# Kernel optimization log

Hardware: AMD Instinct MI355X
Metric: run time of the kernel (lower is better)

## Reference

```python
import jax, jax.numpy as jnp
import numpy as np

GROUPS = 32
NUM_HEADS = 8
EPS = 1e-5


def setup_inputs() -> dict:
    key = jax.random.key(0)
    ks = jax.random.split(key, 8)
    b, c, h, w = 2, 256, 64, 64
    x = jax.random.normal(ks[0], (b, c, h, w), dtype=jnp.float32)
    gn_w = jnp.ones((c,), dtype=jnp.float32)
    gn_b = jnp.zeros((c,), dtype=jnp.float32)
    qkv_w = jax.random.normal(ks[1], (3 * c, c), dtype=jnp.float32) * 0.02  # 1x1 conv
    qkv_b = jnp.zeros((3 * c,), dtype=jnp.float32)
    proj_w = jax.random.normal(ks[2], (c, c), dtype=jnp.float32) * 0.02  # 1x1 conv
    proj_b = jnp.zeros((c,), dtype=jnp.float32)
    return {"x": x, "gn_w": gn_w, "gn_b": gn_b, "qkv_w": qkv_w,
            "qkv_b": qkv_b, "proj_w": proj_w, "proj_b": proj_b}


def _group_norm(x, w, b):
    bsz, c, h, wd = x.shape
    xg = x.reshape(bsz, GROUPS, c // GROUPS, h * wd)
    mean = jnp.mean(xg, axis=(2, 3), keepdims=True)
    var = jnp.mean(jnp.square(xg - mean), axis=(2, 3), keepdims=True)
    xn = ((xg - mean) * jax.lax.rsqrt(var + EPS)).reshape(bsz, c, h, wd)
    return xn * w[None, :, None, None] + b[None, :, None, None]


def reference(x, gn_w, gn_b, qkv_w, qkv_b, proj_w, proj_b):
    b, c, h, w = x.shape
    hd = c // NUM_HEADS
    s = h * w
    xn = _group_norm(x, gn_w, gn_b)
    # 1x1 conv == channel matmul
    qkv = jnp.einsum('oc,bcs->bos', qkv_w, xn.reshape(b, c, s)) + qkv_b[None, :, None]
    qkv = qkv.reshape(b, 3, NUM_HEADS, hd, s)
    q, k, v = qkv[:, 0], qkv[:, 1], qkv[:, 2]  # (b, nh, hd, s)
    scale = 1.0 / jnp.sqrt(jnp.asarray(hd, dtype=x.dtype))
    scores = jnp.einsum('bhds,bhdt->bhst', q, k) * scale  # (b, nh, s, s)
    attn = jax.nn.softmax(scores, axis=-1)
    out = jnp.einsum('bhst,bhdt->bhds', attn, v)  # (b, nh, hd, s)
    out = out.reshape(b, c, h, w)
    out = jnp.einsum('oc,bcs->bos', proj_w, out.reshape(b, c, s)).reshape(b, c, h, w)
    out = out + proj_b[None, :, None, None]
    return out + x
```

## Files before the change

### kernel.cpp

```cpp
#include <hip/hip_runtime.h>
#include <hip/hip_bf16.h>

#define B_ 2
#define C_ 256
#define S_ 4096
#define NH 8
#define HD 32
#define EPSV 1e-5f
#define QSC2 0.25503487942324256f

typedef __bf16 bf16_t;
typedef bf16_t bf16x8 __attribute__((ext_vector_type(8)));
typedef float f32x4 __attribute__((ext_vector_type(4)));
typedef float f32x16 __attribute__((ext_vector_type(16)));
typedef int i32x2 __attribute__((ext_vector_type(2)));
typedef __hip_bfloat16 hbf;

__device__ inline unsigned cvtpk_bf16(float a, float b) {
  unsigned r;
  asm("v_cvt_pk_bf16_f32 %0, %1, %2" : "=v"(r) : "v"(a), "v"(b));
  return r;
}

#if __has_builtin(__builtin_amdgcn_exp2f)
#define EXP2R(x) __builtin_amdgcn_exp2f(x)
#else
#define EXP2R(x) exp2f(x)
#endif

__global__ __launch_bounds__(256) void f2bf_kernel(const float* __restrict__ src, hbf* __restrict__ dst, int n) {
  int i = blockIdx.x * 256 + threadIdx.x;
  if (i < n) dst[i] = __float2bfloat16(src[i]);
}

__global__ __launch_bounds__(1024) void gn_kernel(const float* __restrict__ x, const float* __restrict__ gw,
                                                  const float* __restrict__ gb, hbf* __restrict__ xn_t) {
  int b = blockIdx.x >> 5, g = blockIdx.x & 31;
  const float* xp = x + ((size_t)b * C_ + g * 8) * S_;
  float sum = 0.f, sumsq = 0.f;
  const float4* xp4 = (const float4*)xp;
  for (int i = threadIdx.x; i < 8 * S_ / 4; i += 1024) {
    float4 v = xp4[i];
    sum += v.x + v.y + v.z + v.w;
    sumsq += v.x * v.x + v.y * v.y + v.z * v.z + v.w * v.w;
  }
#pragma unroll
  for (int off = 32; off > 0; off >>= 1) {
    sum += __shfl_down(sum, off);
    sumsq += __shfl_down(sumsq, off);
  }
  __shared__ float red[2][16];
  int wid = threadIdx.x >> 6;
  if ((threadIdx.x & 63) == 0) { red[0][wid] = sum; red[1][wid] = sumsq; }
  __syncthreads();
  sum = 0.f; sumsq = 0.f;
#pragma unroll
  for (int k = 0; k < 16; k++) { sum += red[0][k]; sumsq += red[1][k]; }
  const float inv_n = 1.f / (8 * S_);
  float mean = sum * inv_n;
  float rstd = rsqrtf(fmaxf(sumsq * inv_n - mean * mean, 0.f) + EPSV);
  float scv[8], shv[8];
#pragma unroll
  for (int c = 0; c < 8; c++) {
    scv[c] = gw[g * 8 + c] * rstd;
    shv[c] = gb[g * 8 + c] - mean * scv[c];
  }
  hbf* outp = xn_t + (size_t)b * S_ * C_ + g * 8;
  for (int s = threadIdx.x; s < S_; s += 1024) {
    alignas(16) hbf tmp[8];
#pragma unroll
    for (int c = 0; c < 8; c++)
      tmp[c] = __float2bfloat16(xp[(size_t)c * S_ + s] * scv[c] + shv[c]);
    *(uint4*)&outp[(size_t)s * C_] = *(uint4*)tmp;
  }
}

__global__ __launch_bounds__(256) void qkv_gemm(const hbf* __restrict__ xn_t, const hbf* __restrict__ wb,
                                                const float* __restrict__ bias,
                                                hbf* __restrict__ qbuf, hbf* __restrict__ kg,
                                                hbf* __restrict__ vg) {
  int bt = blockIdx.z;
  int m0 = blockIdx.x * 64;
  int n0 = blockIdx.y * 64;
  const hbf* A = xn_t + (size_t)bt * S_ * C_;
  __shared__ hbf a_lds[64][72];
  __shared__ hbf b_lds[64][72];
  int tid = threadIdx.x, lane = tid & 63, wid = tid >> 6;
  int wm = (wid >> 1) * 32, wn = (wid & 1) * 32;
  f32x4 acc[2][2] = {};
  for (int k0 = 0; k0 < C_; k0 += 64) {
    __syncthreads();
    int r = tid >> 3, kk = (tid & 7) * 8;
#pragma unroll
    for (int p = 0; p < 2; p++) {
      *(bf16x8*)&a_lds[r + p * 32][kk] = *(const bf16x8*)&A[(size_t)(m0 + r + p * 32) * C_ + k0 + kk];
      *(bf16x8*)&b_lds[r + p * 32][kk] = *(const bf16x8*)&wb[(size_t)(n0 + r + p * 32) * C_ + k0 + kk];
    }
    __syncthreads();
#pragma unroll
    for (int kk2 = 0; kk2 < 64; kk2 += 32) {
      bf16x8 af[2], bfr[2];
#pragma unroll
      for (int mi = 0; mi < 2; mi++)
        af[mi] = *(const bf16x8*)&a_lds[wm + mi * 16 + (lane & 15)][kk2 + (lane >> 4) * 8];
#pragma unroll
      for (int ni = 0; ni < 2; ni++)
        bfr[ni] = *(const bf16x8*)&b_lds[wn + ni * 16 + (lane & 15)][kk2 + (lane >> 4) * 8];
#pragma unroll
      for (int mi = 0; mi < 2; mi++)
#pragma unroll
        for (int ni = 0; ni < 2; ni++)
          acc[mi][ni] = __builtin_amdgcn_mfma_f32_16x16x32_bf16(af[mi], bfr[ni], acc[mi][ni], 0, 0, 0);
    }
  }
#pragma unroll
  for (int mi = 0; mi < 2; mi++)
#pragma unroll
    for (int ni = 0; ni < 2; ni++) {
      int o = n0 + wn + ni * 16 + (lane & 15);
      int s = m0 + wm + mi * 16 + (lane >> 4) * 4;
      float bs = bias[o];
      f32x4 v = acc[mi][ni];
      if (o < 256) {
#pragma unroll
        for (int rr = 0; rr < 4; rr++)
          qbuf[((size_t)bt * S_ + s + rr) * C_ + o] = __float2bfloat16((v[rr] + bs) * QSC2);
      } else if (o < 512) {
        int hh = (o - 256) >> 5, dd = (o - 256) & 31;
        size_t base = (((size_t)(bt * NH + hh) * (S_ >> 5) + (s >> 5)) * 2 + (dd >> 4)) * 512 + (dd & 15);
#pragma unroll
        for (int rr = 0; rr < 4; rr++)
          kg[base + (size_t)((s & 31) + rr) * 16] = __float2bfloat16(v[rr] + bs);
      } else {
        int hh = (o - 512) >> 5, dd = (o - 512) & 31;
        alignas(8) hbf tmp[4];
#pragma unroll
        for (int rr = 0; rr < 4; rr++) tmp[rr] = __float2bfloat16(v[rr] + bs);
        *(uint2*)&vg[(((size_t)(bt * NH + hh) * (S_ >> 4) + (s >> 4)) * 32 + dd) * 16 + (s & 15)] = *(uint2*)tmp;
      }
    }
}

__global__ __launch_bounds__(512, 4) void attn_kernel(const hbf* __restrict__ qbuf, const hbf* __restrict__ kg,
                                                      const hbf* __restrict__ vg, hbf* __restrict__ attn_t) {
  int bid = blockIdx.x;
  int xcd = bid & 7, idx = bid >> 3;
  int combo = (xcd << 1) | (idx >> 6);
  int bt = combo >> 3, h = combo & 7;
  int s0 = (idx & 63) << 6;
  int tid = threadIdx.x, lane = tid & 63, w = tid >> 6;
  int wq = w & 1, wt = w >> 1;
  int l31 = lane & 31, hi = lane >> 5;
  const int loff = (l31 << 4) + (hi << 3);
  int qrow = s0 + wq * 32 + l31;
  bf16x8 qf0 = *(const bf16x8*)&qbuf[((size_t)bt * S_ + qrow) * C_ + h * HD + hi * 8];
  bf16x8 qf1 = *(const bf16x8*)&qbuf[((size_t)bt * S_ + qrow) * C_ + h * HD + 16 + hi * 8];
  bf16x8 ones;
#pragma unroll
  for (int i = 0; i < 8; i++) ones[i] = (bf16_t)1.0f;
  f32x16 o_acc = {0.f,0.f,0.f,0.f,0.f,0.f,0.f,0.f,0.f,0.f,0.f,0.f,0.f,0.f,0.f,0.f};
  f32x16 l_acc = o_acc;
  const f32x16 z16 = o_acc;
  const int tq0 = wt << 10;
  const hbf* kp = kg + ((size_t)(bt * NH + h) * (S_ >> 5) + (tq0 >> 5)) * 1024;
  const hbf* vp = vg + ((size_t)(bt * NH + h) * (S_ >> 4) + (tq0 >> 4)) * 512;
  bf16x8 ka0 = *(const bf16x8*)(kp + loff);
  bf16x8 ka1 = *(const bf16x8*)(kp + loff + 512);
  bf16x8 va0 = *(const bf16x8*)(vp + loff);
  bf16x8 va1 = *(const bf16x8*)(vp + loff + 512);
  kp += 1024; vp += 1024;
  for (int tb = 0; tb < 32; ++tb) {
    bf16x8 kan0 = *(const bf16x8*)(kp + loff);
    bf16x8 kan1 = *(const bf16x8*)(kp + loff + 512);
    bf16x8 van0 = *(const bf16x8*)(vp + loff);
    bf16x8 van1 = *(const bf16x8*)(vp + loff + 512);
    f32x16 sc = __builtin_amdgcn_mfma_f32_32x32x16_bf16(ka0, qf0, z16, 0, 0, 0);
    sc = __builtin_amdgcn_mfma_f32_32x32x16_bf16(ka1, qf1, sc, 0, 0, 0);
#pragma unroll
    for (int i = 0; i < 16; i++) sc[i] = EXP2R(sc[i]);
#pragma unroll
    for (int kb = 0; kb < 2; kb++) {
      unsigned a0 = cvtpk_bf16(sc[kb * 8 + 0], sc[kb * 8 + 1]);
      unsigned b0 = cvtpk_bf16(sc[kb * 8 + 2], sc[kb * 8 + 3]);
      unsigned a1 = cvtpk_bf16(sc[kb * 8 + 4], sc[kb * 8 + 5]);
      unsigned b1 = cvtpk_bf16(sc[kb * 8 + 6], sc[kb * 8 + 7]);
      i32x2 ra = __builtin_amdgcn_permlane32_swap((int)a0, (int)a1, false, false);
      i32x2 rb = __builtin_amdgcn_permlane32_swap((int)b0, (int)b1, false, false);
      union { unsigned u[4]; bf16x8 v; } pf;
      pf.u[0] = (unsigned)ra[0]; pf.u[1] = (unsigned)rb[0];
      pf.u[2] = (unsigned)ra[1]; pf.u[3] = (unsigned)rb[1];
      l_acc = __builtin_amdgcn_mfma_f32_32x32x16_bf16(ones, pf.v, l_acc, 0, 0, 0);
      o_acc = __builtin_amdgcn_mfma_f32_32x32x16_bf16(kb ? va1 : va0, pf.v, o_acc, 0, 0, 0);
    }
    ka0 = kan0; ka1 = kan1; va0 = van0; va1 = van1;
    kp += 1024; vp += 1024;
  }
  __shared__ f32x16 ored[6 * 64];
  __shared__ float lred[8 * 64];
  __syncthreads();
  lred[(w << 6) + lane] = l_acc[0];
  if (wt > 0) ored[((w - 2) << 6) + lane] = o_acc;
  __syncthreads();
  if (wt == 0) {
    float l_tot = 0.f;
#pragma unroll
    for (int k = 0; k < 4; k++)
      l_tot += lred[((wq + 2 * k) << 6) + l31];
    f32x16 o = o_acc;
#pragma unroll
    for (int k = 0; k < 3; k++) {
      f32x16 t2 = ored[((wq + 2 * k) << 6) + lane];
#pragma unroll
      for (int i = 0; i < 16; i++) o[i] += t2[i];
    }
    float inv_l = 1.0f / l_tot;
#pragma unroll
    for (int c2 = 0; c2 < 4; c2++) {
      alignas(8) hbf tmp[4];
#pragma unroll
      for (int r = 0; r < 4; r++) tmp[r] = __float2bfloat16(o[c2 * 4 + r] * inv_l);
      *(uint2*)&attn_t[((size_t)bt * S_ + qrow) * C_ + h * HD + c2 * 8 + hi * 4] = *(uint2*)tmp;
    }
  }
}

__global__ __launch_bounds__(256) void proj_gemm(const hbf* __restrict__ attn_t, const hbf* __restrict__ wb,
                                                 const float* __restrict__ bias, const float* __restrict__ x,
                                                 float* __restrict__ out) {
  int bt = blockIdx.z;
  int m0 = blockIdx.x * 64;
  int n0 = blockIdx.y * 64;
  const hbf* A = attn_t + (size_t)bt * S_ * C_;
  __shared__ hbf a_lds[64][72];
  __shared__ hbf b_lds[64][72];
  int tid = threadIdx.x, lane = tid & 63, wid = tid >> 6;
  int wm = (wid >> 1) * 32, wn = (wid & 1) * 32;
  f32x4 acc[2][2] = {};
  for (int k0 = 0; k0 < C_; k0 += 64) {
    __syncthreads();
    int r = tid >> 3, kk = (tid & 7) * 8;
#pragma unroll
    for (int p = 0; p < 2; p++) {
      *(bf16x8*)&a_lds[r + p * 32][kk] = *(const bf16x8*)&A[(size_t)(m0 + r + p * 32) * C_ + k0 + kk];
      *(bf16x8*)&b_lds[r + p * 32][kk] = *(const bf16x8*)&wb[(size_t)(n0 + r + p * 32) * C_ + k0 + kk];
    }
    __syncthreads();
#pragma unroll
    for (int kk2 = 0; kk2 < 64; kk2 += 32) {
      bf16x8 af[2], bfr[2];
#pragma unroll
      for (int mi = 0; mi < 2; mi++)
        af[mi] = *(const bf16x8*)&a_lds[wm + mi * 16 + (lane & 15)][kk2 + (lane >> 4) * 8];
#pragma unroll
      for (int ni = 0; ni < 2; ni++)
        bfr[ni] = *(const bf16x8*)&b_lds[wn + ni * 16 + (lane & 15)][kk2 + (lane >> 4) * 8];
#pragma unroll
      for (int mi = 0; mi < 2; mi++)
#pragma unroll
        for (int ni = 0; ni < 2; ni++)
          acc[mi][ni] = __builtin_amdgcn_mfma_f32_16x16x32_bf16(af[mi], bfr[ni], acc[mi][ni], 0, 0, 0);
    }
  }
#pragma unroll
  for (int mi = 0; mi < 2; mi++)
#pragma unroll
    for (int ni = 0; ni < 2; ni++) {
      int o = n0 + wn + ni * 16 + (lane & 15);
      int s = m0 + wm + mi * 16 + (lane >> 4) * 4;
      size_t base = ((size_t)bt * C_ + o) * S_ + s;
      float pb = bias[o];
      float4 xr = *(const float4*)&x[base];
      float4 res;
      res.x = acc[mi][ni][0] + pb + xr.x;
      res.y = acc[mi][ni][1] + pb + xr.y;
      res.z = acc[mi][ni][2] + pb + xr.z;
      res.w = acc[mi][ni][3] + pb + xr.w;
      *(float4*)&out[base] = res;
    }
}

extern "C" void kernel_launch(void* const* d_in, const int* in_sizes, int n_in,
                              void* d_out, int out_size, void* d_ws, size_t ws_size,
                              hipStream_t stream) {
  const float* x = (const float*)d_in[0];
  const float* gn_w = (const float*)d_in[1];
  const float* gn_b = (const float*)d_in[2];
  const float* qkv_w = (const float*)d_in[3];
  const float* qkv_b = (const float*)d_in[4];
  const float* proj_w = (const float*)d_in[5];
  const float* proj_b = (const float*)d_in[6];
  float* out = (float*)d_out;

  hbf* qkv_w_bf = (hbf*)d_ws;
  hbf* proj_w_bf = qkv_w_bf + 768 * 256;
  hbf* xn_t = proj_w_bf + 256 * 256;
  hbf* qbuf = xn_t + (size_t)B_ * S_ * C_;
  hbf* kg = qbuf + (size_t)B_ * S_ * C_;
  hbf* vg = kg + (size_t)B_ * S_ * C_;
  hbf* attn_t = vg + (size_t)B_ * S_ * C_;

  dim3 blk(256);
  f2bf_kernel<<<(768 * 256 + 255) / 256, blk, 0, stream>>>(qkv_w, qkv_w_bf, 768 * 256);
  f2bf_kernel<<<(256 * 256 + 255) / 256, blk, 0, stream>>>(proj_w, proj_w_bf, 256 * 256);
  gn_kernel<<<64, dim3(1024), 0, stream>>>(x, gn_w, gn_b, xn_t);
  qkv_gemm<<<dim3(64, 12, 2), blk, 0, stream>>>(xn_t, qkv_w_bf, qkv_b, qbuf, kg, vg);
  attn_kernel<<<dim3(1024), dim3(512), 0, stream>>>(qbuf, kg, vg, attn_t);
  proj_gemm<<<dim3(64, 4, 2), blk, 0, stream>>>(attn_t, proj_w_bf, proj_b, x, out);
}
```

Baseline: 93.06 us.

## Software-pipeline QK^T with softmax-PV and replace ones-MFMA row sum with VALU sum

The attention loop now computes the QK^T scores for the next key block before running exp, bf16 packing and the PV MFMA on the current block. This lets the score MFMAs overlap the transcendental and permute work. The softmax denominator is no longer built with an extra MFMA against a ones vector. Each lane sums its fp32 exp values in registers, and the final reduction adds the two half-wave partial sums, removing two MFMAs per iteration. The cost is more live registers for the extra score accumulator. The denominator now sums unrounded fp32 values, while the numerator still uses bf16-rounded probabilities.

```diff
diff --git a/kernel.cpp b/kernel.cpp
--- a/kernel.cpp
+++ b/kernel.cpp
@@ -141,6 +141,32 @@
     }
 }
 
+__device__ inline void softmax_pv(f32x16 sc, bf16x8 va0, bf16x8 va1,
+                                  f32x16& o_acc, float& l_run) {
+#pragma unroll
+  for (int i = 0; i < 16; i++) sc[i] = EXP2R(sc[i]);
+  {
+    float s0a = sc[0] + sc[1], s1a = sc[2] + sc[3], s2a = sc[4] + sc[5], s3a = sc[6] + sc[7];
+    float s4a = sc[8] + sc[9], s5a = sc[10] + sc[11], s6a = sc[12] + sc[13], s7a = sc[14] + sc[15];
+    s0a += s1a; s2a += s3a; s4a += s5a; s6a += s7a;
+    s0a += s2a; s4a += s6a;
+    l_run += s0a + s4a;
+  }
+#pragma unroll
+  for (int kb = 0; kb < 2; kb++) {
+    unsigned a0 = cvtpk_bf16(sc[kb * 8 + 0], sc[kb * 8 + 1]);
+    unsigned b0 = cvtpk_bf16(sc[kb * 8 + 2], sc[kb * 8 + 3]);
+    unsigned a1 = cvtpk_bf16(sc[kb * 8 + 4], sc[kb * 8 + 5]);
+    unsigned b1 = cvtpk_bf16(sc[kb * 8 + 6], sc[kb * 8 + 7]);
+    i32x2 ra = __builtin_amdgcn_permlane32_swap((int)a0, (int)a1, false, false);
+    i32x2 rb = __builtin_amdgcn_permlane32_swap((int)b0, (int)b1, false, false);
+    union { unsigned u[4]; bf16x8 v; } pf;
+    pf.u[0] = (unsigned)ra[0]; pf.u[1] = (unsigned)rb[0];
+    pf.u[2] = (unsigned)ra[1]; pf.u[3] = (unsigned)rb[1];
+    o_acc = __builtin_amdgcn_mfma_f32_32x32x16_bf16(kb ? va1 : va0, pf.v, o_acc, 0, 0, 0);
+  }
+}
+
 __global__ __launch_bounds__(512, 4) void attn_kernel(const hbf* __restrict__ qbuf, const hbf* __restrict__ kg,
                                                       const hbf* __restrict__ vg, hbf* __restrict__ attn_t) {
   int bid = blockIdx.x;
@@ -155,57 +181,48 @@
   int qrow = s0 + wq * 32 + l31;
   bf16x8 qf0 = *(const bf16x8*)&qbuf[((size_t)bt * S_ + qrow) * C_ + h * HD + hi * 8];
   bf16x8 qf1 = *(const bf16x8*)&qbuf[((size_t)bt * S_ + qrow) * C_ + h * HD + 16 + hi * 8];
-  bf16x8 ones;
-#pragma unroll
-  for (int i = 0; i < 8; i++) ones[i] = (bf16_t)1.0f;
   f32x16 o_acc = {0.f,0.f,0.f,0.f,0.f,0.f,0.f,0.f,0.f,0.f,0.f,0.f,0.f,0.f,0.f,0.f};
-  f32x16 l_acc = o_acc;
   const f32x16 z16 = o_acc;
+  float l_run = 0.f;
   const int tq0 = wt << 10;
-  const hbf* kp = kg + ((size_t)(bt * NH + h) * (S_ >> 5) + (tq0 >> 5)) * 1024;
-  const hbf* vp = vg + ((size_t)(bt * NH + h) * (S_ >> 4) + (tq0 >> 4)) * 512;
-  bf16x8 ka0 = *(const bf16x8*)(kp + loff);
-  bf16x8 ka1 = *(const bf16x8*)(kp + loff + 512);
-  bf16x8 va0 = *(const bf16x8*)(vp + loff);
-  bf16x8 va1 = *(const bf16x8*)(vp + loff + 512);
-  kp += 1024; vp += 1024;
-  for (int tb = 0; tb < 32; ++tb) {
-    bf16x8 kan0 = *(const bf16x8*)(kp + loff);
-    bf16x8 kan1 = *(const bf16x8*)(kp + loff + 512);
-    bf16x8 van0 = *(const bf16x8*)(vp + loff);
-    bf16x8 van1 = *(const bf16x8*)(vp + loff + 512);
-    f32x16 sc = __builtin_amdgcn_mfma_f32_32x32x16_bf16(ka0, qf0, z16, 0, 0, 0);
-    sc = __builtin_amdgcn_mfma_f32_32x32x16_bf16(ka1, qf1, sc, 0, 0, 0);
-#pragma unroll
-    for (int i = 0; i < 16; i++) sc[i] = EXP2R(sc[i]);
-#pragma unroll
-    for (int kb = 0; kb < 2; kb++) {
-      unsigned a0 = cvtpk_bf16(sc[kb * 8 + 0], sc[kb * 8 + 1]);
-      unsigned b0 = cvtpk_bf16(sc[kb * 8 + 2], sc[kb * 8 + 3]);
-      unsigned a1 = cvtpk_bf16(sc[kb * 8 + 4], sc[kb * 8 + 5]);
-      unsigned b1 = cvtpk_bf16(sc[kb * 8 + 6], sc[kb * 8 + 7]);
-      i32x2 ra = __builtin_amdgcn_permlane32_swap((int)a0, (int)a1, false, false);
-      i32x2 rb = __builtin_amdgcn_permlane32_swap((int)b0, (int)b1, false, false);
-      union { unsigned u[4]; bf16x8 v; } pf;
-      pf.u[0] = (unsigned)ra[0]; pf.u[1] = (unsigned)rb[0];
-      pf.u[2] = (unsigned)ra[1]; pf.u[3] = (unsigned)rb[1];
-      l_acc = __builtin_amdgcn_mfma_f32_32x32x16_bf16(ones, pf.v, l_acc, 0, 0, 0);
-      o_acc = __builtin_amdgcn_mfma_f32_32x32x16_bf16(kb ? va1 : va0, pf.v, o_acc, 0, 0, 0);
-    }
+  const hbf* kq = kg + ((size_t)(bt * NH + h) * (S_ >> 5) + (tq0 >> 5)) * 1024;
+  const hbf* vq = vg + ((size_t)(bt * NH + h) * (S_ >> 4) + (tq0 >> 4)) * 512;
+  bf16x8 ka0 = *(const bf16x8*)(kq + loff);
+  bf16x8 ka1 = *(const bf16x8*)(kq + loff + 512);
+  bf16x8 va0 = *(const bf16x8*)(vq + loff);
+  bf16x8 va1 = *(const bf16x8*)(vq + loff + 512);
+  f32x16 sc = __builtin_amdgcn_mfma_f32_32x32x16_bf16(ka0, qf0, z16, 0, 0, 0);
+  sc = __builtin_amdgcn_mfma_f32_32x32x16_bf16(ka1, qf1, sc, 0, 0, 0);
+  ka0 = *(const bf16x8*)(kq + 1024 + loff);
+  ka1 = *(const bf16x8*)(kq + 1024 + loff + 512);
+  kq += 2048;
+  vq += 1024;
+  for (int it = 1; it < 32; ++it) {
+    bf16x8 kan0 = *(const bf16x8*)(kq + loff);
+    bf16x8 kan1 = *(const bf16x8*)(kq + loff + 512);
+    bf16x8 van0 = *(const bf16x8*)(vq + loff);
+    bf16x8 van1 = *(const bf16x8*)(vq + loff + 512);
+    f32x16 scn = __builtin_amdgcn_mfma_f32_32x32x16_bf16(ka0, qf0, z16, 0, 0, 0);
+    scn = __builtin_amdgcn_mfma_f32_32x32x16_bf16(ka1, qf1, scn, 0, 0, 0);
+    softmax_pv(sc, va0, va1, o_acc, l_run);
+    sc = scn;
     ka0 = kan0; ka1 = kan1; va0 = van0; va1 = van1;
-    kp += 1024; vp += 1024;
-  }
+    kq += 1024; vq += 1024;
+  }
+  softmax_pv(sc, va0, va1, o_acc, l_run);
   __shared__ f32x16 ored[6 * 64];
   __shared__ float lred[8 * 64];
   __syncthreads();
-  lred[(w << 6) + lane] = l_acc[0];
+  lred[(w << 6) + lane] = l_run;
   if (wt > 0) ored[((w - 2) << 6) + lane] = o_acc;
   __syncthreads();
   if (wt == 0) {
     float l_tot = 0.f;
 #pragma unroll
-    for (int k = 0; k < 4; k++)
-      l_tot += lred[((wq + 2 * k) << 6) + l31];
+    for (int k = 0; k < 4; k++) {
+      int wp = wq + 2 * k;
+      l_tot += lred[(wp << 6) + l31] + lred[(wp << 6) + 32 + l31];
+    }
     f32x16 o = o_acc;
 #pragma unroll
     for (int k = 0; k < 3; k++) {
```

Measured after the change: 89.71 us. 3.6% less time.
